# Performance work log

Measured on AMD Instinct MI355X. Metric: run time of the kernel, lower is better.

The kernel has to match this reference:

```python
import jax, jax.numpy as jnp
import numpy as np

THETA = 10000.0
NUM_HEADS = 16


def _rope_tables(seq_len, d_k, dtype):
    exponent = jnp.arange(d_k // 2, dtype=jnp.float32) * (2.0 / d_k)
    inv_freq = THETA ** (-exponent)                      # (d_k/2,)
    pos = jnp.arange(seq_len, dtype=jnp.float32)
    angles = pos[:, None] * inv_freq[None, :]            # (n, d_k/2)
    return jnp.cos(angles).astype(dtype), jnp.sin(angles).astype(dtype)


def _apply_rope(x, cos, sin):
    # x: (..., n, d_k); interleaved pair convention: pairs are (x[...,2i], x[...,2i+1])
    x1 = x[..., 0::2]
    x2 = x[..., 1::2]
    r1 = x1 * cos - x2 * sin
    r2 = x1 * sin + x2 * cos
    return jnp.stack([r1, r2], axis=-1).reshape(x.shape)


def setup_inputs() -> dict:
    key = jax.random.key(0)
    ks = jax.random.split(key, 5)
    B, N, D = 2, 4096, 1024
    std = (2.0 / (D + D)) ** 0.5
    return {
        "x": jax.random.normal(ks[0], (B, N, D), dtype=jnp.float32),
        "Wq": jax.random.normal(ks[1], (D, D), dtype=jnp.float32) * std,
        "Wk": jax.random.normal(ks[2], (D, D), dtype=jnp.float32) * std,
        "Wv": jax.random.normal(ks[3], (D, D), dtype=jnp.float32) * std,
        "Wo": jax.random.normal(ks[4], (D, D), dtype=jnp.float32) * std,
    }


def reference(x, Wq, Wk, Wv, Wo):
    B, N, D = x.shape
    H = NUM_HEADS
    d_k = D // H

    def proj(W):
        y = jnp.einsum('oi,bni->bno', W, x)
        return y.reshape(B, N, H, d_k).transpose(0, 2, 1, 3)  # (b,h,n,d)

    Q, K, V = proj(Wq), proj(Wk), proj(Wv)

    cos, sin = _rope_tables(N, d_k, x.dtype)
    Q = _apply_rope(Q, cos, sin)
    K = _apply_rope(K, cos, sin)

    scores = jnp.einsum('bhnd,bhmd->bhnm', Q, K) / jnp.sqrt(jnp.asarray(d_k, x.dtype))
    causal = jnp.tril(jnp.ones((N, N), dtype=bool))
    scores = jnp.where(causal, scores, -jnp.inf)
    attn = jax.nn.softmax(scores, axis=-1)
    out = jnp.einsum('bhnm,bhmd->bhnd', attn, V)          # (b,h,n,d)
    out = out.transpose(0, 2, 1, 3).reshape(B, N, D)
    return jnp.einsum('oi,bni->bno', Wo, out)
```

## Files before the change

### kernel.cpp

```cpp
#include <hip/hip_runtime.h>
#include <hip/hip_bf16.h>
#include <stdint.h>

typedef __attribute__((ext_vector_type(8))) short short8;
typedef __attribute__((ext_vector_type(4))) float f32x4;
typedef __attribute__((ext_vector_type(2))) unsigned uint32x2;

#define NSEQ 4096
#define DMODEL 1024
#define MROWS 8192

__device__ __forceinline__ unsigned short f2bf(float f) {
  union { float f; unsigned u; } v; v.f = f;
  unsigned r = v.u + 0x7fffu + ((v.u >> 16) & 1u);
  return (unsigned short)(r >> 16);
}

__device__ __forceinline__ unsigned pkc(float lo, float hi) {
  unsigned r;
  asm("v_cvt_pk_bf16_f32 %0, %1, %2" : "=v"(r) : "v"(lo), "v"(hi));
  return r;
}

__device__ __forceinline__ void gload16(const unsigned short* g, unsigned short* l) {
  __builtin_amdgcn_global_load_lds(
      (const __attribute__((address_space(1))) unsigned int*)g,
      (__attribute__((address_space(3))) unsigned int*)l, 16, 0, 0);
}

__device__ __forceinline__ void pexch(unsigned x, unsigned y, unsigned& w_lo, unsigned& w_hi) {
  uint32x2 t = __builtin_amdgcn_permlane32_swap(x, y, false, false);
  uint32x2 u = __builtin_amdgcn_permlane16_swap(t[0], t[1], false, false);
  w_lo = u[0];
  w_hi = u[1];
}

__global__ void k_prep(const float* __restrict__ x,
                       const float* __restrict__ Wq, const float* __restrict__ Wk,
                       const float* __restrict__ Wv, const float* __restrict__ Wo,
                       unsigned short* __restrict__ xb, unsigned short* __restrict__ Wb,
                       float* __restrict__ cosT, float* __restrict__ sinT) {
  int bid = blockIdx.x;
  if (bid < 8192) {
    int i = (bid * 256 + threadIdx.x) * 4;
    float4 v = *(const float4*)(x + i);
    ushort4 o;
    o.x = f2bf(v.x); o.y = f2bf(v.y); o.z = f2bf(v.z); o.w = f2bf(v.w);
    *(ushort4*)(xb + i) = o;
  } else if (bid < 12288) {
    int r = bid - 8192;
    int z = r >> 10;
    const float* src = (z == 0) ? Wq : (z == 1) ? Wk : (z == 2) ? Wv : Wo;
    float sc = (z == 0) ? 0.18033688011112042f : 1.0f;
    int i = ((r & 1023) * 256 + threadIdx.x) * 4;
    float4 v = *(const float4*)(src + i);
    ushort4 o;
    o.x = f2bf(v.x * sc); o.y = f2bf(v.y * sc); o.z = f2bf(v.z * sc); o.w = f2bf(v.w * sc);
    *(ushort4*)(Wb + (size_t)z * 1048576 + i) = o;
  } else {
    int i = (bid - 12288) * 256 + threadIdx.x;
    int pos = i >> 5, j = i & 31;
    float invf = exp2f(-(float)j * 0.41524101186092029f);
    float ang = (float)pos * invf;
    cosT[i] = cosf(ang);
    sinT[i] = sinf(ang);
  }
}

__global__ __launch_bounds__(256) void k_gemm_bt(
    const unsigned short* __restrict__ A,
    const unsigned short* __restrict__ Bw,
    unsigned short* __restrict__ obf,
    unsigned short* __restrict__ Vt,
    float* __restrict__ of32,
    const float* __restrict__ cosT, const float* __restrict__ sinT,
    int K, int modeArg) {
  const int N = DMODEL;
  const int q8 = gridDim.x >> 3;
  const int wg = (blockIdx.x & 7) * q8 + (blockIdx.x >> 3);
  const int z = wg >> 9;
  const int rr = wg & 511;
  const int bn = rr & 7, bm = rr >> 3;
  const int mode = (modeArg < 0) ? z : modeArg;
  const unsigned short* Bz = Bw + (size_t)z * DMODEL * K;
  unsigned short* oz = (obf && mode <= 1) ? (obf + (size_t)z * MROWS * DMODEL) : nullptr;

  const int t = threadIdx.x;
  const int w = t >> 6, lane = t & 63;
  const int wr = w >> 1, wc = w & 1;
  const int lr = lane & 15, lg = lane >> 4;

  __shared__ __align__(16) unsigned short SM[2][128 * 64];
  unsigned short* Al = SM[0];
  unsigned short* Bl = SM[1];

  const unsigned short* Ab = A + (size_t)bm * 128 * K;
  const unsigned short* Bb = Bz + (size_t)bn * 128 * K;
  const int trow = t >> 3, tcol = (t & 7) * 8;

  f32x4 acc[4][4] = {};

  for (int k0 = 0; k0 < K; k0 += 64) {
#pragma unroll
    for (int c = 0; c < 4; ++c) {
      gload16(Ab + (size_t)(c * 32 + trow) * K + k0 + tcol, &Al[c * 2048 + t * 8]);
      gload16(Bb + (size_t)(c * 32 + trow) * K + k0 + tcol, &Bl[c * 2048 + t * 8]);
    }
    asm volatile("s_waitcnt vmcnt(0)" ::: "memory");
    __syncthreads();
#pragma unroll
    for (int kk = 0; kk < 2; ++kk) {
      short8 af[4], bfr[4];
#pragma unroll
      for (int mi = 0; mi < 4; ++mi)
        af[mi] = *(const short8*)&Al[(wr * 64 + mi * 16 + lr) * 64 + kk * 32 + lg * 8];
#pragma unroll
      for (int ni = 0; ni < 4; ++ni)
        bfr[ni] = *(const short8*)&Bl[(wc * 64 + ni * 16 + lr) * 64 + kk * 32 + lg * 8];
#pragma unroll
      for (int mi = 0; mi < 4; ++mi)
#pragma unroll
        for (int ni = 0; ni < 4; ++ni)
          acc[mi][ni] = __builtin_amdgcn_mfma_f32_16x16x32_bf16(af[mi], bfr[ni], acc[mi][ni], 0, 0, 0);
    }
    __syncthreads();
  }

  if (mode <= 1 || mode == 3) {
    float* Cf = (float*)&SM[0][0];
#pragma unroll
    for (int half = 0; half < 2; ++half) {
      if (half) __syncthreads();
      if (wr == half) {
#pragma unroll
        for (int mi = 0; mi < 4; ++mi)
#pragma unroll
          for (int ni = 0; ni < 4; ++ni)
#pragma unroll
            for (int r = 0; r < 4; ++r) {
              int row = mi * 16 + lg * 4 + r;
              int col = (wc * 64 + ni * 16 + lr) ^ (lg << 3);
              Cf[row * 128 + col] = acc[mi][ni][r];
            }
      }
      __syncthreads();
      int pr = t >> 2;
      int gm = bm * 128 + half * 64 + pr;
      int xorv = ((pr >> 2) & 3) << 3;
      if (mode == 3) {
        float* orow = of32 + (size_t)gm * N + bn * 128;
#pragma unroll
        for (int k = 0; k < 4; ++k) {
          int c0 = (t & 3) * 8 + k * 32;
          int cs = c0 ^ xorv;
          float4 va = *(const float4*)&Cf[pr * 128 + cs];
          float4 vb = *(const float4*)&Cf[pr * 128 + cs + 4];
          *(float4*)(orow + c0) = va;
          *(float4*)(orow + c0 + 4) = vb;
        }
      } else {
        int pos = gm & (NSEQ - 1);
        const float* cB = cosT + pos * 32;
        const float* sB = sinT + pos * 32;
        unsigned short* orow = oz + (size_t)gm * N + bn * 128;
#pragma unroll
        for (int k = 0; k < 4; ++k) {
          int c0 = (t & 3) * 8 + k * 32;
          int cs = c0 ^ xorv;
          float4 va = *(const float4*)&Cf[pr * 128 + cs];
          float4 vb = *(const float4*)&Cf[pr * 128 + cs + 4];
          int j0 = (c0 & 63) >> 1;
          float4 cv = *(const float4*)&cB[j0];
          float4 sv = *(const float4*)&sB[j0];
          uint4 o;
          o.x = pkc(va.x * cv.x - va.y * sv.x, va.x * sv.x + va.y * cv.x);
          o.y = pkc(va.z * cv.y - va.w * sv.y, va.z * sv.y + va.w * cv.y);
          o.z = pkc(vb.x * cv.z - vb.y * sv.z, vb.x * sv.z + vb.y * cv.z);
          o.w = pkc(vb.z * cv.w - vb.w * sv.w, vb.z * sv.w + vb.w * cv.w);
          *(uint4*)(orow + c0) = o;
        }
      }
    }
  } else {
#pragma unroll
    for (int mi = 0; mi < 4; ++mi)
#pragma unroll
      for (int ni = 0; ni < 4; ++ni) {
        int gm0 = bm * 128 + wr * 64 + mi * 16 + lg * 4;
        int gn = bn * 128 + wc * 64 + ni * 16 + lr;
        int b = gm0 >> 12, n = gm0 & (NSEQ - 1);
        int h = gn >> 6, d = gn & 63;
        uint2 u;
        u.x = pkc(acc[mi][ni][0], acc[mi][ni][1]);
        u.y = pkc(acc[mi][ni][2], acc[mi][ni][3]);
        *(uint2*)(Vt + ((size_t)((b * 16 + h) * 64 + d)) * NSEQ + n) = u;
      }
  }
}

__global__ __launch_bounds__(256, 2) void k_attn12(
    const unsigned short* __restrict__ Qb,
    const unsigned short* __restrict__ Kb,
    const unsigned short* __restrict__ Vtg,
    unsigned short* __restrict__ AO) {
  const int id = blockIdx.x;
  const int bh = id & 31;
  const int pq = id >> 5;
  const int b = bh >> 4, h = bh & 15;
  const int t = threadIdx.x;
  const int w = t >> 6, lane = t & 63;
  const int lr = lane & 15, hi4 = lane >> 4;
  const size_t rowbase = (size_t)b * NSEQ;

  __shared__ __align__(16) unsigned short Kl[2][64 * 64];
  __shared__ __align__(16) unsigned short Vl[2][64 * 64];
  __shared__ __align__(16) unsigned short Pl[4][16 * 64];

  const int pswz = (lr & 7) << 3;

  short8 ones;
#pragma unroll
  for (int i = 0; i < 8; ++i) ones[i] = (short)0x3F80;

#define STAGE(buf, kv0)                                                                   \
  {                                                                                       \
    _Pragma("unroll")                                                                     \
    for (int it = 0; it < 2; ++it) {                                                      \
      int c = t + it * 256;                                                               \
      int row = c >> 3, sg = (c & 7) ^ (row & 7);                                         \
      gload16(Kb + (rowbase + (kv0) + row) * DMODEL + h * 64 + sg * 8, &Kl[buf][c * 8]);  \
      gload16(Vtg + ((size_t)bh * 64 + row) * NSEQ + (kv0) + sg * 8, &Vl[buf][c * 8]);    \
    }                                                                                     \
  }

#pragma unroll
  for (int qi = 0; qi < 2; ++qi) {
    const int qt = qi ? pq : (31 - pq);
    const int q0w = qt * 128 + w * 32;

    short8 qf[2][2];
#pragma unroll
    for (int sub = 0; sub < 2; ++sub) {
      const unsigned short* qp = Qb + (rowbase + q0w + sub * 16 + lr) * DMODEL + h * 64 + hi4 * 8;
#pragma unroll
      for (int s = 0; s < 2; ++s)
        qf[sub][s] = *(const short8*)(qp + s * 32);
    }

    f32x4 oacc[2][4] = {};
    f32x4 lacc[2] = {};
    const int nkv = (qt + 1) * 2;

    STAGE(0, 0);
    asm volatile("s_waitcnt vmcnt(0)" ::: "memory");
    __syncthreads();

    for (int ib = 0; ib < nkv; ++ib) {
      const int kv0 = ib * 64, cur = ib & 1;
      if (ib + 1 < nkv) STAGE(cur ^ 1, kv0 + 64);

      if (kv0 <= q0w + 31) {
        short8 Kf[4][2], Vf[2][4];
#pragma unroll
        for (int t4 = 0; t4 < 4; ++t4)
#pragma unroll
          for (int s = 0; s < 2; ++s)
            Kf[t4][s] = *(const short8*)&Kl[cur][(t4 * 16 + lr) * 64 + (((s * 4 + hi4) ^ (lr & 7)) * 8)];
#pragma unroll
        for (int c = 0; c < 2; ++c)
#pragma unroll
          for (int dt = 0; dt < 4; ++dt)
            Vf[c][dt] = *(const short8*)&Vl[cur][(dt * 16 + lr) * 64 + (((c * 4 + hi4) ^ (lr & 7)) * 8)];

#pragma unroll
        for (int sub = 0; sub < 2; ++sub) {
          const int qs = q0w + sub * 16;
          const int qlane = qs + lr;
          f32x4 sa[4];
          const f32x4 zz = {0.f, 0.f, 0.f, 0.f};
          __builtin_amdgcn_s_setprio(1);
#pragma unroll
          for (int t4 = 0; t4 < 4; ++t4) {
            f32x4 x = __builtin_amdgcn_mfma_f32_16x16x32_bf16(Kf[t4][0], qf[sub][0], zz, 0, 0, 0);
            sa[t4] = __builtin_amdgcn_mfma_f32_16x16x32_bf16(Kf[t4][1], qf[sub][1], x, 0, 0, 0);
          }
          __builtin_amdgcn_s_setprio(0);
          if (kv0 + 63 > qs) {
#pragma unroll
            for (int t4 = 0; t4 < 4; ++t4)
#pragma unroll
              for (int r = 0; r < 4; ++r)
                if (kv0 + t4 * 16 + hi4 * 4 + r > qlane) sa[t4][r] = -1e30f;
          }
#pragma unroll
          for (int t4 = 0; t4 < 4; ++t4)
#pragma unroll
            for (int r = 0; r < 4; ++r)
              sa[t4][r] = __builtin_amdgcn_exp2f(sa[t4][r]);

          unsigned a0 = pkc(sa[0][0], sa[0][1]), a1 = pkc(sa[0][2], sa[0][3]);
          unsigned a2 = pkc(sa[1][0], sa[1][1]), a3 = pkc(sa[1][2], sa[1][3]);
          unsigned a4 = pkc(sa[2][0], sa[2][1]), a5 = pkc(sa[2][2], sa[2][3]);
          unsigned a6 = pkc(sa[3][0], sa[3][1]), a7 = pkc(sa[3][2], sa[3][3]);
          unsigned w0, w1, w2, w3, x0, x1, x2, x3;
          pexch(a0, a2, w0, w2);
          pexch(a1, a3, w1, w3);
          pexch(a4, a6, x0, x2);
          pexch(a5, a7, x1, x3);
          union { uint4 u; short8 s; } P0, P1;
          P0.u.x = w0; P0.u.y = w1; P0.u.z = w2; P0.u.w = w3;
          P1.u.x = x0; P1.u.y = x1; P1.u.z = x2; P1.u.w = x3;
          short8 pf0 = P0.s;
          short8 pf1 = P1.s;

          __builtin_amdgcn_s_setprio(1);
#pragma unroll
          for (int dt = 0; dt < 4; ++dt) {
            oacc[sub][dt] = __builtin_amdgcn_mfma_f32_16x16x32_bf16(Vf[0][dt], pf0, oacc[sub][dt], 0, 0, 0);
            oacc[sub][dt] = __builtin_amdgcn_mfma_f32_16x16x32_bf16(Vf[1][dt], pf1, oacc[sub][dt], 0, 0, 0);
          }
          lacc[sub] = __builtin_amdgcn_mfma_f32_16x16x32_bf16(ones, pf0, lacc[sub], 0, 0, 0);
          lacc[sub] = __builtin_amdgcn_mfma_f32_16x16x32_bf16(ones, pf1, lacc[sub], 0, 0, 0);
          __builtin_amdgcn_s_setprio(0);
        }
      }
      asm volatile("s_waitcnt vmcnt(0)" ::: "memory");
      __syncthreads();
    }

#pragma unroll
    for (int sub = 0; sub < 2; ++sub) {
      float inv = 1.f / lacc[sub][0];
#pragma unroll
      for (int dt = 0; dt < 4; ++dt) {
        uint2 u;
        u.x = pkc(oacc[sub][dt][0] * inv, oacc[sub][dt][1] * inv);
        u.y = pkc(oacc[sub][dt][2] * inv, oacc[sub][dt][3] * inv);
        *(uint2*)&Pl[w][lr * 64 + ((dt * 16 + hi4 * 4) ^ pswz)] = u;
      }
      asm volatile("s_waitcnt lgkmcnt(0)" ::: "memory");
      __builtin_amdgcn_sched_barrier(0);
      int q2 = lane >> 2, ch = (lane & 3) * 16;
      int qswz = (q2 & 7) << 3;
      uint4 r0 = *(const uint4*)&Pl[w][q2 * 64 + (ch ^ qswz)];
      uint4 r1 = *(const uint4*)&Pl[w][q2 * 64 + ((ch + 8) ^ qswz)];
      unsigned short* op = AO + (rowbase + q0w + sub * 16 + q2) * DMODEL + h * 64 + ch;
      *(uint4*)op = r0;
      *(uint4*)(op + 8) = r1;
      __syncthreads();
    }
  }
}

extern "C" void kernel_launch(void* const* d_in, const int* in_sizes, int n_in,
                              void* d_out, int out_size, void* d_ws, size_t ws_size,
                              hipStream_t stream) {
  const float* x  = (const float*)d_in[0];
  const float* Wq = (const float*)d_in[1];
  const float* Wk = (const float*)d_in[2];
  const float* Wv = (const float*)d_in[3];
  const float* Wo = (const float*)d_in[4];
  float* out = (float*)d_out;
  char* ws = (char*)d_ws;

  unsigned short* xb  = (unsigned short*)(ws);
  unsigned short* Wb  = (unsigned short*)(ws + 16777216);
  unsigned short* Qb  = (unsigned short*)(ws + 25165824);
  unsigned short* Kb  = Qb + 8388608;
  unsigned short* Vtg = (unsigned short*)(ws + 58720256);
  unsigned short* AO  = (unsigned short*)(ws + 75497472);
  float* cosT = (float*)(ws + 92274688);
  float* sinT = (float*)(ws + 92798976);

  k_prep<<<12800, 256, 0, stream>>>(x, Wq, Wk, Wv, Wo, xb, Wb, cosT, sinT);

  k_gemm_bt<<<1536, 256, 0, stream>>>(xb, Wb, Qb, Vtg, nullptr, cosT, sinT, DMODEL, -1);

  k_attn12<<<512, 256, 0, stream>>>(Qb, Kb, Vtg, AO);

  k_gemm_bt<<<512, 256, 0, stream>>>(AO, Wb + 3145728, nullptr, nullptr, out, cosT, sinT, DMODEL, 3);
}
```

Baseline: 217.1 us.

## Fuse Q, K, V projections into one GEMM kernel sharing the A tile

Replaces the 1536-block QKV GEMM launch with a dedicated 512-block kernel where each block computes Q, K and V tiles for the same 128x128 output region. The x tile is loaded into shared memory once and reused across all three weight matrices, which cuts global and LDS traffic for A threefold. In exchange each thread holds three accumulator sets (48 f32x4), shared memory grows to 64KB, and there are fewer blocks, which lowers parallelism and may raise register pressure or spills despite the launch_bounds hint. The output GEMM is split into a simpler mode-free kernel.

```diff
diff --git a/kernel.cpp b/kernel.cpp
--- a/kernel.cpp
+++ b/kernel.cpp
@@ -67,70 +67,67 @@
   }
 }
 
-__global__ __launch_bounds__(256) void k_gemm_bt(
+__global__ __launch_bounds__(256, 2) void k_gemm_qkv(
     const unsigned short* __restrict__ A,
     const unsigned short* __restrict__ Bw,
     unsigned short* __restrict__ obf,
     unsigned short* __restrict__ Vt,
-    float* __restrict__ of32,
-    const float* __restrict__ cosT, const float* __restrict__ sinT,
-    int K, int modeArg) {
-  const int N = DMODEL;
-  const int q8 = gridDim.x >> 3;
-  const int wg = (blockIdx.x & 7) * q8 + (blockIdx.x >> 3);
-  const int z = wg >> 9;
-  const int rr = wg & 511;
-  const int bn = rr & 7, bm = rr >> 3;
-  const int mode = (modeArg < 0) ? z : modeArg;
-  const unsigned short* Bz = Bw + (size_t)z * DMODEL * K;
-  unsigned short* oz = (obf && mode <= 1) ? (obf + (size_t)z * MROWS * DMODEL) : nullptr;
-
+    const float* __restrict__ cosT, const float* __restrict__ sinT) {
+  const int wg = (blockIdx.x & 7) * 64 + (blockIdx.x >> 3);
+  const int bn = wg & 7, bm = wg >> 3;
   const int t = threadIdx.x;
   const int w = t >> 6, lane = t & 63;
   const int wr = w >> 1, wc = w & 1;
   const int lr = lane & 15, lg = lane >> 4;
 
-  __shared__ __align__(16) unsigned short SM[2][128 * 64];
-  unsigned short* Al = SM[0];
-  unsigned short* Bl = SM[1];
-
-  const unsigned short* Ab = A + (size_t)bm * 128 * K;
-  const unsigned short* Bb = Bz + (size_t)bn * 128 * K;
+  __shared__ __align__(16) unsigned short SM[4][128 * 64];
+
+  const unsigned short* Ab = A + (size_t)bm * 128 * DMODEL;
+  const unsigned short* Bb = Bw + (size_t)bn * 128 * DMODEL;
   const int trow = t >> 3, tcol = (t & 7) * 8;
 
-  f32x4 acc[4][4] = {};
-
-  for (int k0 = 0; k0 < K; k0 += 64) {
+  f32x4 acc[3][4][4] = {};
+
+  for (int k0 = 0; k0 < DMODEL; k0 += 64) {
 #pragma unroll
     for (int c = 0; c < 4; ++c) {
-      gload16(Ab + (size_t)(c * 32 + trow) * K + k0 + tcol, &Al[c * 2048 + t * 8]);
-      gload16(Bb + (size_t)(c * 32 + trow) * K + k0 + tcol, &Bl[c * 2048 + t * 8]);
+      gload16(Ab + (size_t)(c * 32 + trow) * DMODEL + k0 + tcol, &SM[0][c * 2048 + t * 8]);
+#pragma unroll
+      for (int z = 0; z < 3; ++z)
+        gload16(Bb + (size_t)z * 1048576 + (size_t)(c * 32 + trow) * DMODEL + k0 + tcol,
+                &SM[1 + z][c * 2048 + t * 8]);
     }
     asm volatile("s_waitcnt vmcnt(0)" ::: "memory");
     __syncthreads();
 #pragma unroll
     for (int kk = 0; kk < 2; ++kk) {
-      short8 af[4], bfr[4];
+      short8 af[4];
 #pragma unroll
       for (int mi = 0; mi < 4; ++mi)
-        af[mi] = *(const short8*)&Al[(wr * 64 + mi * 16 + lr) * 64 + kk * 32 + lg * 8];
-#pragma unroll
-      for (int ni = 0; ni < 4; ++ni)
-        bfr[ni] = *(const short8*)&Bl[(wc * 64 + ni * 16 + lr) * 64 + kk * 32 + lg * 8];
-#pragma unroll
-      for (int mi = 0; mi < 4; ++mi)
+        af[mi] = *(const short8*)&SM[0][(wr * 64 + mi * 16 + lr) * 64 + kk * 32 + lg * 8];
+#pragma unroll
+      for (int z = 0; z < 3; ++z) {
+        short8 bfr[4];
 #pragma unroll
         for (int ni = 0; ni < 4; ++ni)
-          acc[mi][ni] = __builtin_amdgcn_mfma_f32_16x16x32_bf16(af[mi], bfr[ni], acc[mi][ni], 0, 0, 0);
-    }
-    __syncthreads();
-  }
-
-  if (mode <= 1 || mode == 3) {
-    float* Cf = (float*)&SM[0][0];
+          bfr[ni] = *(const short8*)&SM[1 + z][(wc * 64 + ni * 16 + lr) * 64 + kk * 32 + lg * 8];
+#pragma unroll
+        for (int mi = 0; mi < 4; ++mi)
+#pragma unroll
+          for (int ni = 0; ni < 4; ++ni)
+            acc[z][mi][ni] = __builtin_amdgcn_mfma_f32_16x16x32_bf16(af[mi], bfr[ni], acc[z][mi][ni], 0, 0, 0);
+      }
+    }
+    __syncthreads();
+  }
+
+  float* Cf = (float*)&SM[0][0];
+#pragma unroll
+  for (int z = 0; z < 2; ++z) {
+    unsigned short* oz = obf + (size_t)z * MROWS * DMODEL;
 #pragma unroll
     for (int half = 0; half < 2; ++half) {
-      if (half) __syncthreads();
+      __syncthreads();
       if (wr == half) {
 #pragma unroll
         for (int mi = 0; mi < 4; ++mi)
@@ -140,61 +137,132 @@
             for (int r = 0; r < 4; ++r) {
               int row = mi * 16 + lg * 4 + r;
               int col = (wc * 64 + ni * 16 + lr) ^ (lg << 3);
-              Cf[row * 128 + col] = acc[mi][ni][r];
+              Cf[row * 128 + col] = acc[z][mi][ni][r];
             }
       }
       __syncthreads();
       int pr = t >> 2;
       int gm = bm * 128 + half * 64 + pr;
+      int pos = gm & (NSEQ - 1);
       int xorv = ((pr >> 2) & 3) << 3;
-      if (mode == 3) {
-        float* orow = of32 + (size_t)gm * N + bn * 128;
-#pragma unroll
-        for (int k = 0; k < 4; ++k) {
-          int c0 = (t & 3) * 8 + k * 32;
-          int cs = c0 ^ xorv;
-          float4 va = *(const float4*)&Cf[pr * 128 + cs];
-          float4 vb = *(const float4*)&Cf[pr * 128 + cs + 4];
-          *(float4*)(orow + c0) = va;
-          *(float4*)(orow + c0 + 4) = vb;
-        }
-      } else {
-        int pos = gm & (NSEQ - 1);
-        const float* cB = cosT + pos * 32;
-        const float* sB = sinT + pos * 32;
-        unsigned short* orow = oz + (size_t)gm * N + bn * 128;
-#pragma unroll
-        for (int k = 0; k < 4; ++k) {
-          int c0 = (t & 3) * 8 + k * 32;
-          int cs = c0 ^ xorv;
-          float4 va = *(const float4*)&Cf[pr * 128 + cs];
-          float4 vb = *(const float4*)&Cf[pr * 128 + cs + 4];
-          int j0 = (c0 & 63) >> 1;
-          float4 cv = *(const float4*)&cB[j0];
-          float4 sv = *(const float4*)&sB[j0];
-          uint4 o;
-          o.x = pkc(va.x * cv.x - va.y * sv.x, va.x * sv.x + va.y * cv.x);
-          o.y = pkc(va.z * cv.y - va.w * sv.y, va.z * sv.y + va.w * cv.y);
-          o.z = pkc(vb.x * cv.z - vb.y * sv.z, vb.x * sv.z + vb.y * cv.z);
-          o.w = pkc(vb.z * cv.w - vb.w * sv.w, vb.z * sv.w + vb.w * cv.w);
-          *(uint4*)(orow + c0) = o;
-        }
+      const float* cB = cosT + pos * 32;
+      const float* sB = sinT + pos * 32;
+      unsigned short* orow = oz + (size_t)gm * DMODEL + bn * 128;
+#pragma unroll
+      for (int k = 0; k < 4; ++k) {
+        int c0 = (t & 3) * 8 + k * 32;
+        int cs = c0 ^ xorv;
+        float4 va = *(const float4*)&Cf[pr * 128 + cs];
+        float4 vb = *(const float4*)&Cf[pr * 128 + cs + 4];
+        int j0 = (c0 & 63) >> 1;
+        float4 cv = *(const float4*)&cB[j0];
+        float4 sv = *(const float4*)&sB[j0];
+        uint4 o;
+        o.x = pkc(va.x * cv.x - va.y * sv.x, va.x * sv.x + va.y * cv.x);
+        o.y = pkc(va.z * cv.y - va.w * sv.y, va.z * sv.y + va.w * cv.y);
+        o.z = pkc(vb.x * cv.z - vb.y * sv.z, vb.x * sv.z + vb.y * cv.z);
+        o.w = pkc(vb.z * cv.w - vb.w * sv.w, vb.z * sv.w + vb.w * cv.w);
+        *(uint4*)(orow + c0) = o;
       }
     }
-  } else {
-#pragma unroll
-    for (int mi = 0; mi < 4; ++mi)
-#pragma unroll
-      for (int ni = 0; ni < 4; ++ni) {
-        int gm0 = bm * 128 + wr * 64 + mi * 16 + lg * 4;
-        int gn = bn * 128 + wc * 64 + ni * 16 + lr;
-        int b = gm0 >> 12, n = gm0 & (NSEQ - 1);
-        int h = gn >> 6, d = gn & 63;
-        uint2 u;
-        u.x = pkc(acc[mi][ni][0], acc[mi][ni][1]);
-        u.y = pkc(acc[mi][ni][2], acc[mi][ni][3]);
-        *(uint2*)(Vt + ((size_t)((b * 16 + h) * 64 + d)) * NSEQ + n) = u;
-      }
+  }
+#pragma unroll
+  for (int mi = 0; mi < 4; ++mi)
+#pragma unroll
+    for (int ni = 0; ni < 4; ++ni) {
+      int gm0 = bm * 128 + wr * 64 + mi * 16 + lg * 4;
+      int gn = bn * 128 + wc * 64 + ni * 16 + lr;
+      int b = gm0 >> 12, n = gm0 & (NSEQ - 1);
+      int h = gn >> 6, d = gn & 63;
+      uint2 u;
+      u.x = pkc(acc[2][mi][ni][0], acc[2][mi][ni][1]);
+      u.y = pkc(acc[2][mi][ni][2], acc[2][mi][ni][3]);
+      *(uint2*)(Vt + ((size_t)((b * 16 + h) * 64 + d)) * NSEQ + n) = u;
+    }
+}
+
+__global__ __launch_bounds__(256) void k_gemm_bt(
+    const unsigned short* __restrict__ A,
+    const unsigned short* __restrict__ Bw,
+    float* __restrict__ of32,
+    int K) {
+  const int N = DMODEL;
+  const int q8 = gridDim.x >> 3;
+  const int wg = (blockIdx.x & 7) * q8 + (blockIdx.x >> 3);
+  const int rr = wg & 511;
+  const int bn = rr & 7, bm = rr >> 3;
+
+  const int t = threadIdx.x;
+  const int w = t >> 6, lane = t & 63;
+  const int wr = w >> 1, wc = w & 1;
+  const int lr = lane & 15, lg = lane >> 4;
+
+  __shared__ __align__(16) unsigned short SM[2][128 * 64];
+  unsigned short* Al = SM[0];
+  unsigned short* Bl = SM[1];
+
+  const unsigned short* Ab = A + (size_t)bm * 128 * K;
+  const unsigned short* Bb = Bw + (size_t)bn * 128 * K;
+  const int trow = t >> 3, tcol = (t & 7) * 8;
+
+  f32x4 acc[4][4] = {};
+
+  for (int k0 = 0; k0 < K; k0 += 64) {
+#pragma unroll
+    for (int c = 0; c < 4; ++c) {
+      gload16(Ab + (size_t)(c * 32 + trow) * K + k0 + tcol, &Al[c * 2048 + t * 8]);
+      gload16(Bb + (size_t)(c * 32 + trow) * K + k0 + tcol, &Bl[c * 2048 + t * 8]);
+    }
+    asm volatile("s_waitcnt vmcnt(0)" ::: "memory");
+    __syncthreads();
+#pragma unroll
+    for (int kk = 0; kk < 2; ++kk) {
+      short8 af[4], bfr[4];
+#pragma unroll
+      for (int mi = 0; mi < 4; ++mi)
+        af[mi] = *(const short8*)&Al[(wr * 64 + mi * 16 + lr) * 64 + kk * 32 + lg * 8];
+#pragma unroll
+      for (int ni = 0; ni < 4; ++ni)
+        bfr[ni] = *(const short8*)&Bl[(wc * 64 + ni * 16 + lr) * 64 + kk * 32 + lg * 8];
+#pragma unroll
+      for (int mi = 0; mi < 4; ++mi)
+#pragma unroll
+        for (int ni = 0; ni < 4; ++ni)
+          acc[mi][ni] = __builtin_amdgcn_mfma_f32_16x16x32_bf16(af[mi], bfr[ni], acc[mi][ni], 0, 0, 0);
+    }
+    __syncthreads();
+  }
+
+  float* Cf = (float*)&SM[0][0];
+#pragma unroll
+  for (int half = 0; half < 2; ++half) {
+    if (half) __syncthreads();
+    if (wr == half) {
+#pragma unroll
+      for (int mi = 0; mi < 4; ++mi)
+#pragma unroll
+        for (int ni = 0; ni < 4; ++ni)
+#pragma unroll
+          for (int r = 0; r < 4; ++r) {
+            int row = mi * 16 + lg * 4 + r;
+            int col = (wc * 64 + ni * 16 + lr) ^ (lg << 3);
+            Cf[row * 128 + col] = acc[mi][ni][r];
+          }
+    }
+    __syncthreads();
+    int pr = t >> 2;
+    int gm = bm * 128 + half * 64 + pr;
+    int xorv = ((pr >> 2) & 3) << 3;
+    float* orow = of32 + (size_t)gm * N + bn * 128;
+#pragma unroll
+    for (int k = 0; k < 4; ++k) {
+      int c0 = (t & 3) * 8 + k * 32;
+      int cs = c0 ^ xorv;
+      float4 va = *(const float4*)&Cf[pr * 128 + cs];
+      float4 vb = *(const float4*)&Cf[pr * 128 + cs + 4];
+      *(float4*)(orow + c0) = va;
+      *(float4*)(orow + c0 + 4) = vb;
+    }
   }
 }
 
@@ -374,9 +442,9 @@
 
   k_prep<<<12800, 256, 0, stream>>>(x, Wq, Wk, Wv, Wo, xb, Wb, cosT, sinT);
 
-  k_gemm_bt<<<1536, 256, 0, stream>>>(xb, Wb, Qb, Vtg, nullptr, cosT, sinT, DMODEL, -1);
+  k_gemm_qkv<<<512, 256, 0, stream>>>(xb, Wb, Qb, Vtg, cosT, sinT);
 
   k_attn12<<<512, 256, 0, stream>>>(Qb, Kb, Vtg, AO);
 
-  k_gemm_bt<<<512, 256, 0, stream>>>(AO, Wb + 3145728, nullptr, nullptr, out, cosT, sinT, DMODEL, 3);
-}
+  k_gemm_bt<<<512, 256, 0, stream>>>(AO, Wb + 3145728, out, DMODEL);
+}
```

Result: faster. 191.1 us (-12.0%).
